# Optimization experiments

Hardware: AMD Instinct MI355X
Metric: run time of the kernel (lower is better)

Reference implementation:

```python
import jax, jax.numpy as jnp
import numpy as np

B, L, H, E = 2, 2048, 16, 64
S, D = L, E


def setup_inputs() -> dict:
    key = jax.random.key(0)
    kq, kk, kv = jax.random.split(key, 3)
    queries = jax.random.normal(kq, (B, L, H, E), dtype=jnp.float32)
    keys = jax.random.normal(kk, (B, S, H, E), dtype=jnp.float32)
    values = jax.random.normal(kv, (B, S, H, D), dtype=jnp.float32)
    return {"queries": queries, "keys": keys, "values": values}


def reference(queries, keys, values):
    # FullAttention forward: mask_flag=True, attn_mask=None -> causal mask,
    # scale=None -> 1/sqrt(E), dropout in eval mode (identity).
    Bq, Lq, Hq, Eq = queries.shape
    Sq = values.shape[1]
    scale = 1.0 / jnp.sqrt(jnp.asarray(Eq, dtype=queries.dtype))
    # [B,H,L,S] score matrix, same as torch.einsum('blhe,bshe->bhls', q, k)
    scores = jnp.einsum('blhe,bshe->bhls', queries, keys)
    # TriangularCausalMask: triu(ones, diagonal=1) -> True above diagonal = masked
    causal = jnp.triu(jnp.ones((Lq, Sq), dtype=bool), k=1)
    scores = jnp.where(causal[None, None, :, :], -jnp.inf, scores)
    A = jax.nn.softmax(scale * scores, axis=-1)
    V = jnp.einsum('bhls,bshd->blhd', A, values)
    return V
```

## Files before the change

### kernel.cpp

```cpp
#include <hip/hip_runtime.h>
#include <hip/hip_bf16.h>


#define B_DIM 2
#define L_DIM 2048
#define H_DIM 16
#define E_DIM 64
#define NEG_INF (-1e30f)
#define CAP   16.0f

typedef __attribute__((ext_vector_type(8))) short short8;
typedef __attribute__((ext_vector_type(4))) float ffrag;

static __device__ __forceinline__ short f2bf(float x) {
    __hip_bfloat16 h = __float2bfloat16(x);
    return *reinterpret_cast<short*>(&h);
}
static __device__ __forceinline__ unsigned pk2(float lo, float hi) {
    __hip_bfloat162 h = __float22bfloat162_rn(make_float2(lo, hi));
    return *reinterpret_cast<unsigned*>(&h);
}

__global__ __launch_bounds__(512, 4)
void attn_fused(const float* __restrict__ Q, const float* __restrict__ K,
                const float* __restrict__ V, float* __restrict__ O) {
    const int lid = blockIdx.x;
    const int x   = lid & 7;
    const int i   = lid >> 3;
    const int bh  = x * 4 + (i >> 4);
    const int b   = bh >> 4;
    const int h   = bh & 15;
    const int p   = i & 15;

    const int tid   = threadIdx.x;
    const int wave  = tid >> 6;
    const int grp   = tid >> 8;
    const int qwave = wave & 3;
    const int lane  = tid & 63;
    const int n16   = lane & 15;
    const int quad  = lane >> 4;

    __shared__ alignas(16) short KV[4][4096];
    __shared__ alignas(16) short Pq[12288];
    short* Kt = KV[grp * 2 + 0];
    short* Vt = KV[grp * 2 + 1];

    const float sc = 0.125f * 1.44269504088896340736f;

    short8 qfs[2][2];
#pragma unroll
    for (int sidx = 0; sidx < 2; ++sidx) {
        const int strip = sidx ? (31 - p) : p;
        const int gq = strip * 64 + qwave * 16 + n16;
        const float4* pq = (const float4*)(Q + (((size_t)b * L_DIM + gq) * H_DIM + h) * E_DIM);
#pragma unroll
        for (int kt = 0; kt < 2; ++kt) {
            float4 x0 = pq[kt * 8 + quad * 2];
            float4 x1 = pq[kt * 8 + quad * 2 + 1];
            short8 f;
            f[0] = f2bf(x0.x * sc); f[1] = f2bf(x0.y * sc);
            f[2] = f2bf(x0.z * sc); f[3] = f2bf(x0.w * sc);
            f[4] = f2bf(x1.x * sc); f[5] = f2bf(x1.y * sc);
            f[6] = f2bf(x1.z * sc); f[7] = f2bf(x1.w * sc);
            qfs[sidx][kt] = f;
        }
    }

    const int gtid = tid & 255;
    const int rr  = gtid >> 2;
    const int c2  = gtid & 3;
    const int kOff0 = rr * 64 + (((2 * c2)     ^ (rr & 7)) * 8);
    const int kOff1 = rr * 64 + (((2 * c2 + 1) ^ (rr & 7)) * 8);
    const int kp2 = (gtid & 31) * 2;
    const int c8  = ((gtid >> 5) & 7) * 8;

    float4 kr[4], va[2], vb2[2];

    auto load_tile = [&](int kt0) {
        const float4* kg = (const float4*)(K + (((size_t)b * L_DIM + kt0 + rr) * H_DIM + h) * E_DIM + c2 * 16);
        kr[0] = kg[0]; kr[1] = kg[1]; kr[2] = kg[2]; kr[3] = kg[3];
        const float* vp = V + (((size_t)b * L_DIM + kt0 + kp2) * H_DIM + h) * E_DIM + c8;
        const float4* vga = (const float4*)vp;
        const float4* vgb = (const float4*)(vp + H_DIM * E_DIM);
        va[0]  = vga[0]; va[1]  = vga[1];
        vb2[0] = vgb[0]; vb2[1] = vgb[1];
    };
    auto store_tile = [&]() {
        short8 w0, w1;
        w0[0] = f2bf(kr[0].x); w0[1] = f2bf(kr[0].y); w0[2] = f2bf(kr[0].z); w0[3] = f2bf(kr[0].w);
        w0[4] = f2bf(kr[1].x); w0[5] = f2bf(kr[1].y); w0[6] = f2bf(kr[1].z); w0[7] = f2bf(kr[1].w);
        w1[0] = f2bf(kr[2].x); w1[1] = f2bf(kr[2].y); w1[2] = f2bf(kr[2].z); w1[3] = f2bf(kr[2].w);
        w1[4] = f2bf(kr[3].x); w1[5] = f2bf(kr[3].y); w1[6] = f2bf(kr[3].z); w1[7] = f2bf(kr[3].w);
        *(short8*)&Kt[kOff0] = w0;
        *(short8*)&Kt[kOff1] = w1;
        const float* a0 = (const float*)va;
        const float* b0 = (const float*)vb2;
#pragma unroll
        for (int i2 = 0; i2 < 8; ++i2)
            *(unsigned*)&Vt[(c8 + i2) * 64 + (((kp2 >> 3) ^ i2) * 8) + (kp2 & 7)] = pk2(a0[i2], b0[i2]);
    };

    const int sw  = n16 & 7;
    const int fo0 = (quad ^ sw) * 8;
    const int fo1 = fo0 ^ 32;
    short* pbase = &Pq[wave * 1024 + n16 * 64];

    {
        const int ntA = p + 1;
        if (grp == 0 || ntA > 1) load_tile(grp << 6);
    }

#pragma unroll
    for (int sidx = 0; sidx < 2; ++sidx) {
        const int strip  = sidx ? (31 - p) : p;
        const int q0     = strip * 64;
        const int ntiles = strip + 1;
        const int T      = (ntiles + 1) >> 1;
        const short8 qf0 = qfs[sidx][0];
        const short8 qf1 = qfs[sidx][1];

        ffrag Oa[4];
#pragma unroll
        for (int nt = 0; nt < 4; ++nt) Oa[nt] = ffrag{0.f, 0.f, 0.f, 0.f};
        float l = 0.f;

        for (int t = 0; t < T; ++t) {
            const int it     = 2 * t + grp;
            const bool valid = (it < ntiles);
            __syncthreads();
            if (valid) store_tile();
            __syncthreads();
            if (it + 2 < ntiles) load_tile((it + 2) << 6);

            if (valid) {
                ffrag S[4];
                __builtin_amdgcn_s_setprio(1);
#pragma unroll
                for (int mt = 0; mt < 4; ++mt) {
                    const int rb = (mt * 16 + n16) * 64;
                    short8 a0 = *(const short8*)&Kt[rb + fo0];
                    short8 a1 = *(const short8*)&Kt[rb + fo1];
                    ffrag z = ffrag{0.f, 0.f, 0.f, 0.f};
                    z = __builtin_amdgcn_mfma_f32_16x16x32_bf16(a0, qf0, z, 0, 0, 0);
                    S[mt] = __builtin_amdgcn_mfma_f32_16x16x32_bf16(a1, qf1, z, 0, 0, 0);
                }
                __builtin_amdgcn_s_setprio(0);

                const bool domask = (it == ntiles - 1);
                float ps = 0.f;
#pragma unroll
                for (int mt = 0; mt < 4; ++mt) {
                    float pv[4];
#pragma unroll
                    for (int r = 0; r < 4; ++r) {
                        float sv = S[mt][r];
                        if (domask && (mt * 16 + quad * 4 + r > qwave * 16 + n16)) sv = NEG_INF;
                        pv[r] = exp2f(sv - CAP);
                        ps += pv[r];
                    }
                    uint2 w;
                    w.x = pk2(pv[0], pv[1]);
                    w.y = pk2(pv[2], pv[3]);
                    *(uint2*)&pbase[(((2 * mt + (quad >> 1)) ^ sw) * 8) + (quad & 1) * 4] = w;
                }
                ps += __shfl_xor(ps, 16);
                ps += __shfl_xor(ps, 32);
                l += ps;

                short8 pa0 = *(const short8*)&pbase[fo0];
                short8 pa1 = *(const short8*)&pbase[fo1];

                __builtin_amdgcn_s_setprio(1);
#pragma unroll
                for (int nt = 0; nt < 4; ++nt) {
                    const int rb = (nt * 16 + n16) * 64;
                    short8 b0 = *(const short8*)&Vt[rb + fo0];
                    short8 b1 = *(const short8*)&Vt[rb + fo1];
                    Oa[nt] = __builtin_amdgcn_mfma_f32_16x16x32_bf16(pa0, b0, Oa[nt], 0, 0, 0);
                    Oa[nt] = __builtin_amdgcn_mfma_f32_16x16x32_bf16(pa1, b1, Oa[nt], 0, 0, 0);
                }
                __builtin_amdgcn_s_setprio(0);
            }
        }

        if (sidx == 0) load_tile(grp << 6);

        __syncthreads();
        float* fO = (float*)&KV[0][0];
        float* fL = (float*)&KV[2][0];
        if (grp == 1) {
            ffrag* dst = (ffrag*)(fO + ((qwave * 64 + lane) << 4));
#pragma unroll
            for (int nt = 0; nt < 4; ++nt) dst[nt] = Oa[nt];
            fL[qwave * 64 + lane] = l;
        }
        __syncthreads();
        if (grp == 0) {
            const ffrag* src = (const ffrag*)(fO + ((qwave * 64 + lane) << 4));
#pragma unroll
            for (int nt = 0; nt < 4; ++nt) Oa[nt] += src[nt];
            l += fL[qwave * 64 + lane];

#pragma unroll
            for (int r = 0; r < 4; ++r) {
                float li  = __shfl(l, quad * 4 + r);
                float inv = 1.0f / li;
                const int row = q0 + qwave * 16 + quad * 4 + r;
                float* op = O + (((size_t)b * L_DIM + row) * H_DIM + h) * E_DIM;
#pragma unroll
                for (int nt = 0; nt < 4; ++nt) op[nt * 16 + n16] = Oa[nt][r] * inv;
            }
        }
    }
}

extern "C" void kernel_launch(void* const* d_in, const int* in_sizes, int n_in,
                              void* d_out, int out_size, void* d_ws, size_t ws_size,
                              hipStream_t stream) {
    const float* Q = (const float*)d_in[0];
    const float* K = (const float*)d_in[1];
    const float* V = (const float*)d_in[2];
    float* O = (float*)d_out;
    attn_fused<<<dim3(512), 512, 0, stream>>>(Q, K, V, O);
}
```

Baseline: 149.9 us.

## Switch attention to 32x32x16 MFMA with register-resident P via permlane32 swap

Replaces the 16x16x32 MFMA tiling with 32x32x16 bf16 MFMAs, splitting each 64x64 tile among four waves as query-half by key-half. The softmax probabilities stay in registers, rearranged with v_permlane32_swap instead of a round trip through shared memory. Fully masked quadrants on the diagonal tile are skipped. Other changes: per-thread K/V pointers and V store offsets are precomputed, Q is loaded per strip instead of upfront, and exp2 uses the hardware builtin. The final reduction now needs two extra barriers to combine the key-half partial sums through shared memory.

```diff
diff --git a/kernel.cpp b/kernel.cpp
--- a/kernel.cpp
+++ b/kernel.cpp
@@ -9,16 +9,20 @@
 #define NEG_INF (-1e30f)
 #define CAP   16.0f
 
-typedef __attribute__((ext_vector_type(8))) short short8;
-typedef __attribute__((ext_vector_type(4))) float ffrag;
-
-static __device__ __forceinline__ short f2bf(float x) {
-    __hip_bfloat16 h = __float2bfloat16(x);
-    return *reinterpret_cast<short*>(&h);
-}
+typedef __attribute__((ext_vector_type(8)))  short    short8;
+typedef __attribute__((ext_vector_type(16))) float    f32x16;
+typedef __attribute__((ext_vector_type(4)))  unsigned u32x4;
+
 static __device__ __forceinline__ unsigned pk2(float lo, float hi) {
     __hip_bfloat162 h = __float22bfloat162_rn(make_float2(lo, hi));
     return *reinterpret_cast<unsigned*>(&h);
+}
+static __device__ __forceinline__ float fexp2(float x) {
+#if __has_builtin(__builtin_amdgcn_exp2f)
+    return __builtin_amdgcn_exp2f(x);
+#else
+    return exp2f(x);
+#endif
 }
 
 __global__ __launch_bounds__(512, 4)
@@ -32,39 +36,21 @@
     const int h   = bh & 15;
     const int p   = i & 15;
 
-    const int tid   = threadIdx.x;
-    const int wave  = tid >> 6;
-    const int grp   = tid >> 8;
-    const int qwave = wave & 3;
-    const int lane  = tid & 63;
-    const int n16   = lane & 15;
-    const int quad  = lane >> 4;
-
-    __shared__ alignas(16) short KV[4][4096];
-    __shared__ alignas(16) short Pq[12288];
+    const int tid  = threadIdx.x;
+    const int wave = tid >> 6;
+    const int grp  = wave >> 2;
+    const int qh   = (wave >> 1) & 1;
+    const int kh   = wave & 1;
+    const int lane = tid & 63;
+    const int l31  = lane & 31;
+    const int hh   = lane >> 5;
+
+    __shared__ short KV[4][4096];
+    __shared__ float lbufRaw[512 + 5632];
     short* Kt = KV[grp * 2 + 0];
     short* Vt = KV[grp * 2 + 1];
 
     const float sc = 0.125f * 1.44269504088896340736f;
-
-    short8 qfs[2][2];
-#pragma unroll
-    for (int sidx = 0; sidx < 2; ++sidx) {
-        const int strip = sidx ? (31 - p) : p;
-        const int gq = strip * 64 + qwave * 16 + n16;
-        const float4* pq = (const float4*)(Q + (((size_t)b * L_DIM + gq) * H_DIM + h) * E_DIM);
-#pragma unroll
-        for (int kt = 0; kt < 2; ++kt) {
-            float4 x0 = pq[kt * 8 + quad * 2];
-            float4 x1 = pq[kt * 8 + quad * 2 + 1];
-            short8 f;
-            f[0] = f2bf(x0.x * sc); f[1] = f2bf(x0.y * sc);
-            f[2] = f2bf(x0.z * sc); f[3] = f2bf(x0.w * sc);
-            f[4] = f2bf(x1.x * sc); f[5] = f2bf(x1.y * sc);
-            f[6] = f2bf(x1.z * sc); f[7] = f2bf(x1.w * sc);
-            qfs[sidx][kt] = f;
-        }
-    }
 
     const int gtid = tid & 255;
     const int rr  = gtid >> 2;
@@ -73,42 +59,38 @@
     const int kOff1 = rr * 64 + (((2 * c2 + 1) ^ (rr & 7)) * 8);
     const int kp2 = (gtid & 31) * 2;
     const int c8  = ((gtid >> 5) & 7) * 8;
+    int vOff[8];
+#pragma unroll
+    for (int j = 0; j < 8; ++j)
+        vOff[j] = (c8 + j) * 64 + (((kp2 >> 3) ^ j) * 8) + (kp2 & 7);
+
+    const float* Kthr = K + (((size_t)b * L_DIM + rr)  * H_DIM + h) * E_DIM + c2 * 16;
+    const float* Vthr = V + (((size_t)b * L_DIM + kp2) * H_DIM + h) * E_DIM + c8;
 
     float4 kr[4], va[2], vb2[2];
 
     auto load_tile = [&](int kt0) {
-        const float4* kg = (const float4*)(K + (((size_t)b * L_DIM + kt0 + rr) * H_DIM + h) * E_DIM + c2 * 16);
+        const float4* kg = (const float4*)(Kthr + (size_t)kt0 * (H_DIM * E_DIM));
         kr[0] = kg[0]; kr[1] = kg[1]; kr[2] = kg[2]; kr[3] = kg[3];
-        const float* vp = V + (((size_t)b * L_DIM + kt0 + kp2) * H_DIM + h) * E_DIM + c8;
+        const float* vp = Vthr + (size_t)kt0 * (H_DIM * E_DIM);
         const float4* vga = (const float4*)vp;
         const float4* vgb = (const float4*)(vp + H_DIM * E_DIM);
         va[0]  = vga[0]; va[1]  = vga[1];
         vb2[0] = vgb[0]; vb2[1] = vgb[1];
     };
     auto store_tile = [&]() {
-        short8 w0, w1;
-        w0[0] = f2bf(kr[0].x); w0[1] = f2bf(kr[0].y); w0[2] = f2bf(kr[0].z); w0[3] = f2bf(kr[0].w);
-        w0[4] = f2bf(kr[1].x); w0[5] = f2bf(kr[1].y); w0[6] = f2bf(kr[1].z); w0[7] = f2bf(kr[1].w);
-        w1[0] = f2bf(kr[2].x); w1[1] = f2bf(kr[2].y); w1[2] = f2bf(kr[2].z); w1[3] = f2bf(kr[2].w);
-        w1[4] = f2bf(kr[3].x); w1[5] = f2bf(kr[3].y); w1[6] = f2bf(kr[3].z); w1[7] = f2bf(kr[3].w);
-        *(short8*)&Kt[kOff0] = w0;
-        *(short8*)&Kt[kOff1] = w1;
+        u32x4 w0 = { pk2(kr[0].x, kr[0].y), pk2(kr[0].z, kr[0].w),
+                     pk2(kr[1].x, kr[1].y), pk2(kr[1].z, kr[1].w) };
+        u32x4 w1 = { pk2(kr[2].x, kr[2].y), pk2(kr[2].z, kr[2].w),
+                     pk2(kr[3].x, kr[3].y), pk2(kr[3].z, kr[3].w) };
+        *(u32x4*)&Kt[kOff0] = w0;
+        *(u32x4*)&Kt[kOff1] = w1;
         const float* a0 = (const float*)va;
         const float* b0 = (const float*)vb2;
 #pragma unroll
-        for (int i2 = 0; i2 < 8; ++i2)
-            *(unsigned*)&Vt[(c8 + i2) * 64 + (((kp2 >> 3) ^ i2) * 8) + (kp2 & 7)] = pk2(a0[i2], b0[i2]);
+        for (int j = 0; j < 8; ++j)
+            *(unsigned*)&Vt[vOff[j]] = pk2(a0[j], b0[j]);
     };
-
-    const int sw  = n16 & 7;
-    const int fo0 = (quad ^ sw) * 8;
-    const int fo1 = fo0 ^ 32;
-    short* pbase = &Pq[wave * 1024 + n16 * 64];
-
-    {
-        const int ntA = p + 1;
-        if (grp == 0 || ntA > 1) load_tile(grp << 6);
-    }
 
 #pragma unroll
     for (int sidx = 0; sidx < 2; ++sidx) {
@@ -116,13 +98,28 @@
         const int q0     = strip * 64;
         const int ntiles = strip + 1;
         const int T      = (ntiles + 1) >> 1;
-        const short8 qf0 = qfs[sidx][0];
-        const short8 qf1 = qfs[sidx][1];
-
-        ffrag Oa[4];
-#pragma unroll
-        for (int nt = 0; nt < 4; ++nt) Oa[nt] = ffrag{0.f, 0.f, 0.f, 0.f};
+
+        short8 qf[4];
+        {
+            const int gq = q0 + qh * 32 + l31;
+            const float* qp = Q + (((size_t)b * L_DIM + gq) * H_DIM + h) * E_DIM + hh * 8;
+#pragma unroll
+            for (int e = 0; e < 4; ++e) {
+                const float4* q4 = (const float4*)(qp + e * 16);
+                float4 x0 = q4[0], x1 = q4[1];
+                u32x4 w = { pk2(x0.x * sc, x0.y * sc), pk2(x0.z * sc, x0.w * sc),
+                            pk2(x1.x * sc, x1.y * sc), pk2(x1.z * sc, x1.w * sc) };
+                qf[e] = __builtin_bit_cast(short8, w);
+            }
+        }
+
+        f32x16 Oa[2];
+        Oa[0] = f32x16{}; Oa[1] = f32x16{};
         float l = 0.f;
+
+        if (sidx == 0) {
+            if (grp == 0 || ntiles > 1) load_tile(grp << 6);
+        }
 
         for (int t = 0; t < T; ++t) {
             const int it     = 2 * t + grp;
@@ -133,82 +130,113 @@
             if (it + 2 < ntiles) load_tile((it + 2) << 6);
 
             if (valid) {
-                ffrag S[4];
-                __builtin_amdgcn_s_setprio(1);
-#pragma unroll
-                for (int mt = 0; mt < 4; ++mt) {
-                    const int rb = (mt * 16 + n16) * 64;
-                    short8 a0 = *(const short8*)&Kt[rb + fo0];
-                    short8 a1 = *(const short8*)&Kt[rb + fo1];
-                    ffrag z = ffrag{0.f, 0.f, 0.f, 0.f};
-                    z = __builtin_amdgcn_mfma_f32_16x16x32_bf16(a0, qf0, z, 0, 0, 0);
-                    S[mt] = __builtin_amdgcn_mfma_f32_16x16x32_bf16(a1, qf1, z, 0, 0, 0);
+                const bool diag = (it == ntiles - 1);
+                if (!(diag && (kh > qh))) {
+                    f32x16 S = f32x16{};
+                    __builtin_amdgcn_s_setprio(1);
+#pragma unroll
+                    for (int e = 0; e < 4; ++e) {
+                        short8 a = *(const short8*)&Kt[(kh * 32 + l31) * 64 +
+                                                       (((e * 2 + hh) ^ (l31 & 7)) * 8)];
+                        S = __builtin_amdgcn_mfma_f32_32x32x16_bf16(a, qf[e], S, 0, 0, 0);
+                    }
+                    __builtin_amdgcn_s_setprio(0);
+
+                    if (diag && kh == qh) {
+#pragma unroll
+                        for (int r = 0; r < 16; ++r) {
+                            const int kloc = (r & 3) + 8 * (r >> 2) + 4 * hh;
+                            if (kloc > l31) S[r] = NEG_INF;
+                        }
+                    }
+
+                    float ps = 0.f;
+#pragma unroll
+                    for (int r = 0; r < 16; ++r) {
+                        S[r] = fexp2(S[r] - CAP);
+                        ps += S[r];
+                    }
+                    ps += __shfl_xor(ps, 32);
+                    l += ps;
+
+                    unsigned c0 = pk2(S[0],  S[1]),  c1 = pk2(S[2],  S[3]);
+                    unsigned c2w = pk2(S[4], S[5]),  c3 = pk2(S[6],  S[7]);
+                    unsigned c4 = pk2(S[8],  S[9]),  c5 = pk2(S[10], S[11]);
+                    unsigned c6 = pk2(S[12], S[13]), c7 = pk2(S[14], S[15]);
+                    asm("v_permlane32_swap_b32 %0, %1" : "+v"(c0), "+v"(c2w));
+                    asm("v_permlane32_swap_b32 %0, %1" : "+v"(c1), "+v"(c3));
+                    asm("v_permlane32_swap_b32 %0, %1" : "+v"(c4), "+v"(c6));
+                    asm("v_permlane32_swap_b32 %0, %1" : "+v"(c5), "+v"(c7));
+                    u32x4 pw0 = { c0, c1, c2w, c3 };
+                    u32x4 pw1 = { c4, c5, c6,  c7 };
+                    short8 pf0 = __builtin_bit_cast(short8, pw0);
+                    short8 pf1 = __builtin_bit_cast(short8, pw1);
+
+                    __builtin_amdgcn_s_setprio(1);
+#pragma unroll
+                    for (int db = 0; db < 2; ++db) {
+                        short8 v0 = *(const short8*)&Vt[(db * 32 + l31) * 64 +
+                                                        (((kh * 4 + 0 + hh) ^ (l31 & 7)) * 8)];
+                        Oa[db] = __builtin_amdgcn_mfma_f32_32x32x16_bf16(pf0, v0, Oa[db], 0, 0, 0);
+                        short8 v1 = *(const short8*)&Vt[(db * 32 + l31) * 64 +
+                                                        (((kh * 4 + 2 + hh) ^ (l31 & 7)) * 8)];
+                        Oa[db] = __builtin_amdgcn_mfma_f32_32x32x16_bf16(pf1, v1, Oa[db], 0, 0, 0);
+                    }
+                    __builtin_amdgcn_s_setprio(0);
                 }
-                __builtin_amdgcn_s_setprio(0);
-
-                const bool domask = (it == ntiles - 1);
-                float ps = 0.f;
-#pragma unroll
-                for (int mt = 0; mt < 4; ++mt) {
-                    float pv[4];
-#pragma unroll
-                    for (int r = 0; r < 4; ++r) {
-                        float sv = S[mt][r];
-                        if (domask && (mt * 16 + quad * 4 + r > qwave * 16 + n16)) sv = NEG_INF;
-                        pv[r] = exp2f(sv - CAP);
-                        ps += pv[r];
-                    }
-                    uint2 w;
-                    w.x = pk2(pv[0], pv[1]);
-                    w.y = pk2(pv[2], pv[3]);
-                    *(uint2*)&pbase[(((2 * mt + (quad >> 1)) ^ sw) * 8) + (quad & 1) * 4] = w;
-                }
-                ps += __shfl_xor(ps, 16);
-                ps += __shfl_xor(ps, 32);
-                l += ps;
-
-                short8 pa0 = *(const short8*)&pbase[fo0];
-                short8 pa1 = *(const short8*)&pbase[fo1];
-
-                __builtin_amdgcn_s_setprio(1);
-#pragma unroll
-                for (int nt = 0; nt < 4; ++nt) {
-                    const int rb = (nt * 16 + n16) * 64;
-                    short8 b0 = *(const short8*)&Vt[rb + fo0];
-                    short8 b1 = *(const short8*)&Vt[rb + fo1];
-                    Oa[nt] = __builtin_amdgcn_mfma_f32_16x16x32_bf16(pa0, b0, Oa[nt], 0, 0, 0);
-                    Oa[nt] = __builtin_amdgcn_mfma_f32_16x16x32_bf16(pa1, b1, Oa[nt], 0, 0, 0);
-                }
-                __builtin_amdgcn_s_setprio(0);
             }
         }
 
         if (sidx == 0) load_tile(grp << 6);
 
         __syncthreads();
-        float* fO = (float*)&KV[0][0];
-        float* fL = (float*)&KV[2][0];
-        if (grp == 1) {
-            ffrag* dst = (ffrag*)(fO + ((qwave * 64 + lane) << 4));
-#pragma unroll
-            for (int nt = 0; nt < 4; ++nt) dst[nt] = Oa[nt];
-            fL[qwave * 64 + lane] = l;
-        }
-        __syncthreads();
-        if (grp == 0) {
-            const ffrag* src = (const ffrag*)(fO + ((qwave * 64 + lane) << 4));
-#pragma unroll
-            for (int nt = 0; nt < 4; ++nt) Oa[nt] += src[nt];
-            l += fL[qwave * 64 + lane];
-
-#pragma unroll
-            for (int r = 0; r < 4; ++r) {
-                float li  = __shfl(l, quad * 4 + r);
-                float inv = 1.0f / li;
-                const int row = q0 + qwave * 16 + quad * 4 + r;
-                float* op = O + (((size_t)b * L_DIM + row) * H_DIM + h) * E_DIM;
-#pragma unroll
-                for (int nt = 0; nt < 4; ++nt) op[nt * 16 + n16] = Oa[nt][r] * inv;
+        float* regf = (float*)&KV[(wave >> 1) & 3][0];
+        float* lb   = lbufRaw;
+        if (kh == 1) {
+#pragma unroll
+            for (int db = 0; db < 2; ++db)
+#pragma unroll
+                for (int r = 0; r < 16; ++r)
+                    regf[(db * 16 + r) * 64 + lane] = Oa[db][r];
+            if (lane < 32) lb[wave * 64 + l31] = l;
+        }
+        __syncthreads();
+        if (kh == 0) {
+#pragma unroll
+            for (int db = 0; db < 2; ++db)
+#pragma unroll
+                for (int r = 0; r < 16; ++r)
+                    Oa[db][r] += regf[(db * 16 + r) * 64 + lane];
+            l += lb[(wave + 1) * 64 + l31];
+        }
+        __syncthreads();
+        if (kh == 0 && grp == 1) {
+#pragma unroll
+            for (int db = 0; db < 2; ++db)
+#pragma unroll
+                for (int r = 0; r < 16; ++r)
+                    regf[(db * 16 + r) * 64 + lane] = Oa[db][r];
+            if (lane < 32) lb[wave * 64 + l31] = l;
+        }
+        __syncthreads();
+        if (kh == 0 && grp == 0) {
+            float* srcf = (float*)&KV[(wave >> 1) + 2][0];
+#pragma unroll
+            for (int db = 0; db < 2; ++db)
+#pragma unroll
+                for (int r = 0; r < 16; ++r)
+                    Oa[db][r] += srcf[(db * 16 + r) * 64 + lane];
+            l += lb[(wave + 4) * 64 + l31];
+
+            const float inv = 1.0f / l;
+#pragma unroll
+            for (int r = 0; r < 16; ++r) {
+                const int rloc = (r & 3) + 8 * (r >> 2) + 4 * hh;
+                const float ir = __shfl(inv, rloc);
+                const int qrow = q0 + qh * 32 + rloc;
+                float* op = O + (((size_t)b * L_DIM + qrow) * H_DIM + h) * E_DIM;
+                op[l31]      = Oa[0][r] * ir;
+                op[32 + l31] = Oa[1][r] * ir;
             }
         }
     }
```

After: 166.9 us. 11.3% more time.
